# Optimization experiments

Measured on AMD Instinct MI355X. Metric: run time of the kernel, lower is better.

## Reference

```python
import jax, jax.numpy as jnp
import numpy as np

DIM = 1024
HEADS = 16


def setup_inputs() -> dict:
    key = jax.random.key(0)
    ks = jax.random.split(key, 8)
    b, n, d = 2, 2048, DIM
    x = jax.random.normal(ks[0], (b, n, d), dtype=jnp.float32)
    # Linear(dim, 3*dim, bias=False): weight stored as [dim, 3*dim] (pre-transposed)
    W_qkv = jax.random.normal(ks[1], (d, 3 * d), dtype=jnp.float32) * (d ** -0.5)
    # Linear(dim, dim) with bias
    W_out = jax.random.normal(ks[2], (d, d), dtype=jnp.float32) * (d ** -0.5)
    b_out = jnp.zeros((d,), dtype=jnp.float32)
    alpha = jnp.ones((1,), dtype=jnp.float32)
    beta = jnp.zeros((1,), dtype=jnp.float32) + 0.5  # nonzero so softmax path is exercised
    gamma = jnp.zeros((1,), dtype=jnp.float32) + 0.1
    return {"x": x, "W_qkv": W_qkv, "W_out": W_out, "b_out": b_out,
            "alpha": alpha, "beta": beta, "gamma": gamma}


def reference(x, W_qkv, W_out, b_out, alpha, beta, gamma):
    b, n, d = x.shape
    h = HEADS
    hd = d // h
    scale = d ** -0.5  # note: full dim, as in the original module
    qkv = x @ W_qkv  # [b, n, 3d]
    q, k, v = jnp.split(qkv, 3, axis=-1)
    # [b, n, d] -> [b, h, n, hd]
    to_heads = lambda t: t.reshape(b, n, h, hd).transpose(0, 2, 1, 3)
    q, k, v = to_heads(q), to_heads(k), to_heads(v)
    dots = jnp.einsum("bhqd,bhkd->bhqk", q, k) * scale  # [b, h, n, n]
    attn = (alpha[0] * jnp.eye(n, dtype=x.dtype)
            + beta[0] * jax.nn.softmax(dots, axis=-1)
            - gamma[0] / n)
    out = jnp.einsum("bhqk,bhkd->bhqd", attn, v)  # [b, h, n, hd]
    out = out.transpose(0, 2, 1, 3).reshape(b, n, d)
    return out @ W_out + b_out
```

## Files before the change

kernel.cpp:

```cpp
#include <hip/hip_runtime.h>
#include <hip/hip_bf16.h>

#define DEVI __device__ __forceinline__

typedef __attribute__((ext_vector_type(8))) short bf16x8;
typedef __attribute__((ext_vector_type(4))) short bf16x4;
typedef __attribute__((ext_vector_type(4))) float f32x4;

DEVI unsigned short f2bf(float f) {
    unsigned u = __float_as_uint(f);
    u += 0x7FFF + ((u >> 16) & 1);
    return (unsigned short)(u >> 16);
}
DEVI float bf2f(unsigned short h) {
    return __uint_as_float(((unsigned)h) << 16);
}
DEVI f32x4 mfma16(bf16x8 a, bf16x8 b, f32x4 c) {
    return __builtin_amdgcn_mfma_f32_16x16x32_bf16(a, b, c, 0, 0, 0);
}
DEVI void gload_lds16(const void* g, void* l) {
    __builtin_amdgcn_global_load_lds(
        (const __attribute__((address_space(1))) unsigned int*)g,
        (__attribute__((address_space(3))) unsigned int*)l, 16, 0, 0);
}

DEVI void wt_body(const float* __restrict__ W, unsigned short* __restrict__ Wt,
                  int N, int n0, int k0, float sc, int tid,
                  unsigned short (*T)[72])
{
#pragma unroll
    for (int j = 0; j < 4; ++j) {
        int idx = tid + j * 256;
        int kk = idx >> 4, c4 = (idx & 15) << 2;
        float4 v = *(const float4*)(W + (size_t)(k0 + kk) * N + n0 + c4);
        T[c4 + 0][kk] = f2bf(v.x * sc); T[c4 + 1][kk] = f2bf(v.y * sc);
        T[c4 + 2][kk] = f2bf(v.z * sc); T[c4 + 3][kk] = f2bf(v.w * sc);
    }
    __syncthreads();
#pragma unroll
    for (int j = 0; j < 4; ++j) {
        int idx = tid + j * 256;
        int n = idx >> 4, c4 = (idx & 15) << 2;
        *(bf16x4*)(Wt + (size_t)(n0 + n) * 1024 + k0 + c4) = *(bf16x4*)&T[n][c4];
    }
}

__global__ __launch_bounds__(256) void k_prep(
    const float* __restrict__ X, const float* __restrict__ Wqkv,
    const float* __restrict__ Wout,
    unsigned short* __restrict__ Xb, unsigned short* __restrict__ Wt1,
    unsigned short* __restrict__ Wt2)
{
    __shared__ unsigned short T[64][72];
    const int tid = threadIdx.x;
    const int bid = blockIdx.x;
    const float QSC = 1.4426950408889634f / 32.0f;
    if (bid < 1024) {
        int i = bid * 256 + tid;
#pragma unroll
        for (int j = 0; j < 4; ++j) {
            int idx = i + j * 262144;
            float4 v = *(const float4*)(X + (size_t)idx * 4);
            bf16x4 hv;
            hv[0] = (short)f2bf(v.x); hv[1] = (short)f2bf(v.y);
            hv[2] = (short)f2bf(v.z); hv[3] = (short)f2bf(v.w);
            *(bf16x4*)(Xb + (size_t)idx * 4) = hv;
        }
    } else if (bid < 1792) {
        int idx = bid - 1024;
        int n0 = (idx % 48) * 64, k0 = (idx / 48) * 64;
        wt_body(Wqkv, Wt1, 3072, n0, k0, (n0 < 1024) ? QSC : 1.0f, tid, T);
    } else {
        int idx = bid - 1792;
        int n0 = (idx & 15) * 64, k0 = (idx >> 4) * 64;
        wt_body(Wout, Wt2, 1024, n0, k0, 1.0f, tid, T);
    }
}

__global__ __launch_bounds__(256) void k_gemm1(
    const unsigned short* __restrict__ A, const unsigned short* __restrict__ B,
    unsigned short* __restrict__ C)
{
    __shared__ unsigned short As[128 * 64];
    __shared__ unsigned short Bs[128 * 64];
    const int tid = threadIdx.x, lane = tid & 63, wid = tid >> 6;
    const int wr = (wid >> 1) * 64, wc = (wid & 1) * 64;
    const int row0 = blockIdx.y * 128, col0 = blockIdx.x * 128;
    const int rsel = lane & 15, kgr = (lane >> 4) * 8;
    const int lr = lane >> 3, lc = (lane & 7) * 8;

    f32x4 acc[4][4];
#pragma unroll
    for (int i = 0; i < 4; ++i)
#pragma unroll
        for (int j = 0; j < 4; ++j) acc[i][j] = (f32x4){0.f, 0.f, 0.f, 0.f};

    for (int k0 = 0; k0 < 1024; k0 += 64) {
        __syncthreads();
#pragma unroll
        for (int i = 0; i < 4; ++i) {
            int rb = wid * 32 + i * 8;
            gload_lds16(A + (size_t)(row0 + rb + lr) * 1024 + k0 + lc, As + rb * 64);
            gload_lds16(B + (size_t)(col0 + rb + lr) * 1024 + k0 + lc, Bs + rb * 64);
        }
        __syncthreads();
#pragma unroll
        for (int ks = 0; ks < 2; ++ks) {
            bf16x8 a[4], b[4];
            int ko = ks * 32 + kgr;
#pragma unroll
            for (int mi = 0; mi < 4; ++mi)
                a[mi] = *(const bf16x8*)(As + (wr + mi * 16 + rsel) * 64 + ko);
#pragma unroll
            for (int nj = 0; nj < 4; ++nj)
                b[nj] = *(const bf16x8*)(Bs + (wc + nj * 16 + rsel) * 64 + ko);
#pragma unroll
            for (int mi = 0; mi < 4; ++mi)
#pragma unroll
                for (int nj = 0; nj < 4; ++nj)
                    acc[mi][nj] = mfma16(a[mi], b[nj], acc[mi][nj]);
        }
    }
    const int rbase = row0 + wr + ((lane >> 4) << 2);
    const int cbase = col0 + wc + rsel;
#pragma unroll
    for (int mi = 0; mi < 4; ++mi)
#pragma unroll
        for (int nj = 0; nj < 4; ++nj)
#pragma unroll
            for (int r = 0; r < 4; ++r)
                C[(size_t)(rbase + mi * 16 + r) * 3072 + cbase + nj * 16] =
                    f2bf(acc[mi][nj][r]);
}

__global__ __launch_bounds__(256) void k_vt(
    const unsigned short* __restrict__ qkv, unsigned short* __restrict__ Vt,
    float* __restrict__ vsum)
{
    __shared__ unsigned short T[64][72];
    __shared__ float ps[64];
    const int tid = threadIdx.x, lane = tid & 63, wid = tid >> 6;
    const int bh = blockIdx.y, b = bh >> 4, h = bh & 15;
    const int n0 = blockIdx.x * 64;
    const unsigned short* src = qkv + (size_t)(b * 2048 + n0) * 3072 + 2048 + h * 64;
#pragma unroll
    for (int j = 0; j < 2; ++j) {
        int idx = tid + j * 256;
        int n = idx >> 3, c8 = (idx & 7) << 3;
        *(bf16x8*)&T[n][c8] = *(const bf16x8*)(src + (size_t)n * 3072 + c8);
    }
    if (tid < 64) ps[tid] = 0.f;
    __syncthreads();
#pragma unroll
    for (int i = 0; i < 16; ++i) {
        int dv = wid * 16 + i;
        Vt[((size_t)bh * 64 + dv) * 2048 + n0 + lane] = T[lane][dv];
    }
    {
        const int col = tid & 63, qtr = tid >> 6;
        float s = 0.f;
#pragma unroll
        for (int i = 0; i < 16; ++i) s += bf2f(T[qtr * 16 + i][col]);
        atomicAdd(&ps[col], s);
        __syncthreads();
        if (tid < 64) atomicAdd(&vsum[bh * 64 + tid], ps[tid]);
    }
}

__global__ __launch_bounds__(256) void k_attn(
    const unsigned short* __restrict__ qkv, const unsigned short* __restrict__ Vt,
    const float* __restrict__ vsum,
    const float* __restrict__ alpha_p, const float* __restrict__ beta_p,
    const float* __restrict__ gamma_p,
    unsigned short* __restrict__ AO)
{
    __shared__ unsigned short Ks[2][64][64];
    __shared__ unsigned short Vs[2][64][64];
    __shared__ unsigned short Ps[4][32][64];
    const int tid = threadIdx.x, lane = tid & 63, wid = tid >> 6;
    const int swz = (blockIdx.x & 7) * 64 + (blockIdx.x >> 3);
    const int bh = swz >> 4, qtb = swz & 15;
    const int b = bh >> 4, h = bh & 15;
    const int q0 = qtb * 128;
    const int rsel = lane & 15, g = lane >> 4;
    const int g4 = g << 2;
    const int wq0 = wid * 32;
    const int r7 = rsel & 7;

    bf16x8 bq[2][2];
#pragma unroll
    for (int qt = 0; qt < 2; ++qt) {
        const unsigned short* qrow =
            qkv + (size_t)(b * 2048 + q0 + wq0 + qt * 16 + rsel) * 3072 + h * 64;
        bq[qt][0] = *(const bf16x8*)(qrow + g * 8);
        bq[qt][1] = *(const bf16x8*)(qrow + 32 + g * 8);
    }

    const int sr = lane >> 3;
    const int ss = (lane & 7) ^ sr;
    const int rb0 = wid * 16, rb1 = wid * 16 + 8;
    const unsigned short* kp0 = qkv + (size_t)(b * 2048) * 3072 + 1024 + h * 64
                              + (size_t)(rb0 + sr) * 3072 + ss * 8;
    const unsigned short* kp1 = kp0 + (size_t)8 * 3072;
    const unsigned short* vp0 = Vt + (size_t)bh * 64 * 2048
                              + (size_t)(rb0 + sr) * 2048 + ss * 8;
    const unsigned short* vp1 = vp0 + (size_t)8 * 2048;
    const size_t KADV = (size_t)64 * 3072;

    f32x4 o[2][4], ol[2];
#pragma unroll
    for (int qt = 0; qt < 2; ++qt) {
#pragma unroll
        for (int dj = 0; dj < 4; ++dj) o[qt][dj] = (f32x4){0.f, 0.f, 0.f, 0.f};
        ol[qt] = (f32x4){0.f, 0.f, 0.f, 0.f};
    }
    bf16x8 ones;
#pragma unroll
    for (int e = 0; e < 8; ++e) ones[e] = (short)0x3F80;

    gload_lds16(kp0, &Ks[0][rb0][0]); gload_lds16(kp1, &Ks[0][rb1][0]);
    gload_lds16(vp0, &Vs[0][rb0][0]); gload_lds16(vp1, &Vs[0][rb1][0]);
    kp0 += KADV; kp1 += KADV; vp0 += 64; vp1 += 64;
    asm volatile("s_waitcnt vmcnt(0)" ::: "memory");
    __syncthreads();

#define BODY(CUR, NXT, DOPF)                                                   \
    {                                                                          \
        if (DOPF) {                                                            \
            gload_lds16(kp0, &Ks[NXT][rb0][0]);                                \
            gload_lds16(kp1, &Ks[NXT][rb1][0]);                                \
            gload_lds16(vp0, &Vs[NXT][rb0][0]);                                \
            gload_lds16(vp1, &Vs[NXT][rb1][0]);                                \
            kp0 += KADV; kp1 += KADV; vp0 += 64; vp1 += 64;                    \
        }                                                                      \
        f32x4 s[2][4];                                                         \
        _Pragma("unroll")                                                      \
        for (int qt = 0; qt < 2; ++qt)                                         \
            _Pragma("unroll")                                                  \
            for (int kj = 0; kj < 4; ++kj)                                     \
                s[qt][kj] = (f32x4){0.f, 0.f, 0.f, 0.f};                       \
        __builtin_amdgcn_s_setprio(1);                                         \
        _Pragma("unroll")                                                      \
        for (int ks = 0; ks < 2; ++ks) {                                       \
            const int sl = ((ks * 4 + g) ^ r7) * 8;                            \
            bf16x8 ak[4];                                                      \
            _Pragma("unroll")                                                  \
            for (int kj = 0; kj < 4; ++kj)                                     \
                ak[kj] = *(const bf16x8*)(&Ks[CUR][kj * 16 + rsel][sl]);       \
            _Pragma("unroll")                                                  \
            for (int qt = 0; qt < 2; ++qt)                                     \
                _Pragma("unroll")                                              \
                for (int kj = 0; kj < 4; ++kj)                                 \
                    s[qt][kj] = mfma16(ak[kj], bq[qt][ks], s[qt][kj]);         \
        }                                                                      \
        __builtin_amdgcn_s_setprio(0);                                         \
        _Pragma("unroll")                                                      \
        for (int qt = 0; qt < 2; ++qt)                                         \
            _Pragma("unroll")                                                  \
            for (int kj = 0; kj < 4; ++kj) {                                   \
                float p0 = __builtin_amdgcn_exp2f(s[qt][kj][0]);               \
                float p1 = __builtin_amdgcn_exp2f(s[qt][kj][1]);               \
                float p2 = __builtin_amdgcn_exp2f(s[qt][kj][2]);               \
                float p3 = __builtin_amdgcn_exp2f(s[qt][kj][3]);               \
                union { __hip_bfloat162 h2[2]; uint2 u; } pk;                  \
                pk.h2[0] = __float22bfloat162_rn(make_float2(p0, p1));         \
                pk.h2[1] = __float22bfloat162_rn(make_float2(p2, p3));         \
                const int slot16 = (kj * 2 + (g >> 1)) ^ r7;                   \
                *(uint2*)(&Ps[wid][qt * 16 + rsel][slot16 * 8 + (g & 1) * 4])  \
                    = pk.u;                                                    \
            }                                                                  \
        __builtin_amdgcn_s_setprio(1);                                         \
        _Pragma("unroll")                                                      \
        for (int ks = 0; ks < 2; ++ks) {                                       \
            const int sl = ((ks * 4 + g) ^ r7) * 8;                            \
            bf16x8 pa0 = *(const bf16x8*)(&Ps[wid][rsel][sl]);                 \
            bf16x8 pa1 = *(const bf16x8*)(&Ps[wid][16 + rsel][sl]);            \
            bf16x8 vb[4];                                                      \
            _Pragma("unroll")                                                  \
            for (int dj = 0; dj < 4; ++dj)                                     \
                vb[dj] = *(const bf16x8*)(&Vs[CUR][dj * 16 + rsel][sl]);       \
            _Pragma("unroll")                                                  \
            for (int dj = 0; dj < 4; ++dj) {                                   \
                o[0][dj] = mfma16(pa0, vb[dj], o[0][dj]);                      \
                o[1][dj] = mfma16(pa1, vb[dj], o[1][dj]);                      \
            }                                                                  \
            ol[0] = mfma16(pa0, ones, ol[0]);                                  \
            ol[1] = mfma16(pa1, ones, ol[1]);                                  \
        }                                                                      \
        __builtin_amdgcn_s_setprio(0);                                         \
        asm volatile("s_waitcnt vmcnt(0)" ::: "memory");                       \
        __syncthreads();                                                       \
    }

#pragma unroll 1
    for (int i = 0; i < 16; ++i) {
        BODY(0, 1, true);
        BODY(1, 0, (i < 15));
    }
#undef BODY

    const float alpha = *alpha_p, beta = *beta_p;
    const float gn = (*gamma_p) / 2048.0f;
#pragma unroll
    for (int qt = 0; qt < 2; ++qt) {
        float linv[4];
#pragma unroll
        for (int r = 0; r < 4; ++r)
            linv[r] = beta / ol[qt][r];
#pragma unroll
        for (int dj = 0; dj < 4; ++dj)
#pragma unroll
            for (int r = 0; r < 4; ++r) {
                int qrow = q0 + wq0 + qt * 16 + g4 + r;
                int dv = dj * 16 + rsel;
                float ov = o[qt][dj][r] * linv[r];
                float vdiag = bf2f(qkv[(size_t)(b * 2048 + qrow) * 3072 + 2048 + h * 64 + dv]);
                float vs = vsum[bh * 64 + dv];
                float res = ov + alpha * vdiag - gn * vs;
                AO[(size_t)(b * 2048 + qrow) * 1024 + h * 64 + dv] = f2bf(res);
            }
    }
}

__global__ __launch_bounds__(256) void k_gemm2(
    const unsigned short* __restrict__ A, const unsigned short* __restrict__ B,
    const float* __restrict__ bias, float* __restrict__ Out)
{
    __shared__ unsigned short As[64 * 64];
    __shared__ unsigned short Bs[128 * 64];
    const int tid = threadIdx.x, lane = tid & 63, wid = tid >> 6;
    const int wr = (wid >> 1) * 32, wc = (wid & 1) * 64;
    const int row0 = blockIdx.y * 64, col0 = blockIdx.x * 128;
    const int rsel = lane & 15, kgr = (lane >> 4) * 8;
    const int lr = lane >> 3, lc = (lane & 7) * 8;

    f32x4 acc[2][4];
#pragma unroll
    for (int i = 0; i < 2; ++i)
#pragma unroll
        for (int j = 0; j < 4; ++j) acc[i][j] = (f32x4){0.f, 0.f, 0.f, 0.f};

    for (int k0 = 0; k0 < 1024; k0 += 64) {
        __syncthreads();
#pragma unroll
        for (int i = 0; i < 2; ++i) {
            int rb = wid * 8 + i * 32;
            gload_lds16(A + (size_t)(row0 + rb + lr) * 1024 + k0 + lc, As + rb * 64);
        }
#pragma unroll
        for (int i = 0; i < 4; ++i) {
            int rb = wid * 8 + i * 32;
            gload_lds16(B + (size_t)(col0 + rb + lr) * 1024 + k0 + lc, Bs + rb * 64);
        }
        __syncthreads();
#pragma unroll
        for (int ks = 0; ks < 2; ++ks) {
            bf16x8 a[2], b[4];
            int ko = ks * 32 + kgr;
#pragma unroll
            for (int mi = 0; mi < 2; ++mi)
                a[mi] = *(const bf16x8*)(As + (wr + mi * 16 + rsel) * 64 + ko);
#pragma unroll
            for (int nj = 0; nj < 4; ++nj)
                b[nj] = *(const bf16x8*)(Bs + (wc + nj * 16 + rsel) * 64 + ko);
#pragma unroll
            for (int mi = 0; mi < 2; ++mi)
#pragma unroll
                for (int nj = 0; nj < 4; ++nj)
                    acc[mi][nj] = mfma16(a[mi], b[nj], acc[mi][nj]);
        }
    }
    const int rbase = row0 + wr + ((lane >> 4) << 2);
    const int cbase = col0 + wc + rsel;
#pragma unroll
    for (int mi = 0; mi < 2; ++mi)
#pragma unroll
        for (int nj = 0; nj < 4; ++nj) {
            int gc = cbase + nj * 16;
            float bv = bias[gc];
#pragma unroll
            for (int r = 0; r < 4; ++r)
                Out[(size_t)(rbase + mi * 16 + r) * 1024 + gc] = acc[mi][nj][r] + bv;
        }
}

extern "C" void kernel_launch(void* const* d_in, const int* in_sizes, int n_in,
                              void* d_out, int out_size, void* d_ws, size_t ws_size,
                              hipStream_t stream) {
    const float* x     = (const float*)d_in[0];
    const float* Wqkv  = (const float*)d_in[1];
    const float* Wout  = (const float*)d_in[2];
    const float* bout  = (const float*)d_in[3];
    const float* alpha = (const float*)d_in[4];
    const float* beta  = (const float*)d_in[5];
    const float* gamma = (const float*)d_in[6];
    float* out = (float*)d_out;

    char* ws = (char*)d_ws;
    unsigned short* Xb  = (unsigned short*)(ws);
    unsigned short* Wt1 = (unsigned short*)(ws + 8388608);
    unsigned short* Wt2 = (unsigned short*)(ws + 14680064);
    unsigned short* qkv = (unsigned short*)(ws + 16777216);
    unsigned short* Vt  = (unsigned short*)(ws + 41943040);
    float* vsum         = (float*)(ws + 50331648);
    unsigned short* AO  = Xb;

    hipMemsetAsync(vsum, 0, 2048 * sizeof(float), stream);
    k_prep<<<2048, 256, 0, stream>>>(x, Wqkv, Wout, Xb, Wt1, Wt2);
    k_gemm1<<<dim3(24, 32), 256, 0, stream>>>(Xb, Wt1, qkv);
    k_vt<<<dim3(32, 32), 256, 0, stream>>>(qkv, Vt, vsum);
    k_attn<<<512, 256, 0, stream>>>(qkv, Vt, vsum, alpha, beta, gamma, AO);
    k_gemm2<<<dim3(8, 64), 256, 0, stream>>>(AO, Wt2, bout, out);
}
```

Measured before the change: 144.1 us.

## Process two KV tiles per barrier in attention and stage GEMM output via LDS

The attention loop now uses four K/V LDS buffers and handles two 64-key tiles per iteration. Both QK products are issued before both exp/PV phases, which halves the number of waitcnt+barrier points and gives more independent MFMA work to hide latency. Separately, the QKV GEMM epilogue writes its accumulators into padded shared memory and then stores 16-byte rows to global, replacing scattered 2-byte stores. The cost is doubled K/V shared memory and more live score registers, which may reduce occupancy.

```diff
diff --git a/kernel.cpp b/kernel.cpp
--- a/kernel.cpp
+++ b/kernel.cpp
@@ -81,8 +81,9 @@
     const unsigned short* __restrict__ A, const unsigned short* __restrict__ B,
     unsigned short* __restrict__ C)
 {
-    __shared__ unsigned short As[128 * 64];
-    __shared__ unsigned short Bs[128 * 64];
+    __shared__ unsigned short Sh[18432];
+    unsigned short* As = Sh;
+    unsigned short* Bs = Sh + 8192;
     const int tid = threadIdx.x, lane = tid & 63, wid = tid >> 6;
     const int wr = (wid >> 1) * 64, wc = (wid & 1) * 64;
     const int row0 = blockIdx.y * 128, col0 = blockIdx.x * 128;
@@ -121,16 +122,23 @@
                     acc[mi][nj] = mfma16(a[mi], b[nj], acc[mi][nj]);
         }
     }
-    const int rbase = row0 + wr + ((lane >> 4) << 2);
-    const int cbase = col0 + wc + rsel;
+    __syncthreads();
+    unsigned short (*wb)[72] = (unsigned short (*)[72])(Sh + wid * 4608);
+    const int g4 = (lane >> 4) << 2;
 #pragma unroll
     for (int mi = 0; mi < 4; ++mi)
 #pragma unroll
         for (int nj = 0; nj < 4; ++nj)
 #pragma unroll
             for (int r = 0; r < 4; ++r)
-                C[(size_t)(rbase + mi * 16 + r) * 3072 + cbase + nj * 16] =
-                    f2bf(acc[mi][nj][r]);
+                wb[mi * 16 + g4 + r][nj * 16 + rsel] = f2bf(acc[mi][nj][r]);
+#pragma unroll
+    for (int rr = 0; rr < 8; ++rr) {
+        int row = rr * 8 + (lane >> 3);
+        int c8 = (lane & 7) * 8;
+        bf16x8 v = *(const bf16x8*)&wb[row][c8];
+        *(bf16x8*)(C + (size_t)(row0 + wr + row) * 3072 + col0 + wc + c8) = v;
+    }
 }
 
 __global__ __launch_bounds__(256) void k_vt(
@@ -174,8 +182,8 @@
     const float* __restrict__ gamma_p,
     unsigned short* __restrict__ AO)
 {
-    __shared__ unsigned short Ks[2][64][64];
-    __shared__ unsigned short Vs[2][64][64];
+    __shared__ unsigned short Ks[4][64][64];
+    __shared__ unsigned short Vs[4][64][64];
     __shared__ unsigned short Ps[4][32][64];
     const int tid = threadIdx.x, lane = tid & 63, wid = tid >> 6;
     const int swz = (blockIdx.x & 7) * 64 + (blockIdx.x >> 3);
@@ -218,27 +226,26 @@
 #pragma unroll
     for (int e = 0; e < 8; ++e) ones[e] = (short)0x3F80;
 
-    gload_lds16(kp0, &Ks[0][rb0][0]); gload_lds16(kp1, &Ks[0][rb1][0]);
-    gload_lds16(vp0, &Vs[0][rb0][0]); gload_lds16(vp1, &Vs[0][rb1][0]);
-    kp0 += KADV; kp1 += KADV; vp0 += 64; vp1 += 64;
+#define STAGE(BUF)                                                             \
+    {                                                                          \
+        gload_lds16(kp0, &Ks[BUF][rb0][0]);                                    \
+        gload_lds16(kp1, &Ks[BUF][rb1][0]);                                    \
+        gload_lds16(vp0, &Vs[BUF][rb0][0]);                                    \
+        gload_lds16(vp1, &Vs[BUF][rb1][0]);                                    \
+        kp0 += KADV; kp1 += KADV; vp0 += 64; vp1 += 64;                        \
+    }
+
+    STAGE(0); STAGE(1);
     asm volatile("s_waitcnt vmcnt(0)" ::: "memory");
     __syncthreads();
 
-#define BODY(CUR, NXT, DOPF)                                                   \
+#define QK(CUR, S)                                                             \
     {                                                                          \
-        if (DOPF) {                                                            \
-            gload_lds16(kp0, &Ks[NXT][rb0][0]);                                \
-            gload_lds16(kp1, &Ks[NXT][rb1][0]);                                \
-            gload_lds16(vp0, &Vs[NXT][rb0][0]);                                \
-            gload_lds16(vp1, &Vs[NXT][rb1][0]);                                \
-            kp0 += KADV; kp1 += KADV; vp0 += 64; vp1 += 64;                    \
-        }                                                                      \
-        f32x4 s[2][4];                                                         \
         _Pragma("unroll")                                                      \
         for (int qt = 0; qt < 2; ++qt)                                         \
             _Pragma("unroll")                                                  \
             for (int kj = 0; kj < 4; ++kj)                                     \
-                s[qt][kj] = (f32x4){0.f, 0.f, 0.f, 0.f};                       \
+                S[qt][kj] = (f32x4){0.f, 0.f, 0.f, 0.f};                       \
         __builtin_amdgcn_s_setprio(1);                                         \
         _Pragma("unroll")                                                      \
         for (int ks = 0; ks < 2; ++ks) {                                       \
@@ -251,17 +258,21 @@
             for (int qt = 0; qt < 2; ++qt)                                     \
                 _Pragma("unroll")                                              \
                 for (int kj = 0; kj < 4; ++kj)                                 \
-                    s[qt][kj] = mfma16(ak[kj], bq[qt][ks], s[qt][kj]);         \
+                    S[qt][kj] = mfma16(ak[kj], bq[qt][ks], S[qt][kj]);         \
         }                                                                      \
         __builtin_amdgcn_s_setprio(0);                                         \
+    }
+
+#define EPV(CUR, S)                                                            \
+    {                                                                          \
         _Pragma("unroll")                                                      \
         for (int qt = 0; qt < 2; ++qt)                                         \
             _Pragma("unroll")                                                  \
             for (int kj = 0; kj < 4; ++kj) {                                   \
-                float p0 = __builtin_amdgcn_exp2f(s[qt][kj][0]);               \
-                float p1 = __builtin_amdgcn_exp2f(s[qt][kj][1]);               \
-                float p2 = __builtin_amdgcn_exp2f(s[qt][kj][2]);               \
-                float p3 = __builtin_amdgcn_exp2f(s[qt][kj][3]);               \
+                float p0 = __builtin_amdgcn_exp2f(S[qt][kj][0]);               \
+                float p1 = __builtin_amdgcn_exp2f(S[qt][kj][1]);               \
+                float p2 = __builtin_amdgcn_exp2f(S[qt][kj][2]);               \
+                float p3 = __builtin_amdgcn_exp2f(S[qt][kj][3]);               \
                 union { __hip_bfloat162 h2[2]; uint2 u; } pk;                  \
                 pk.h2[0] = __float22bfloat162_rn(make_float2(p0, p1));         \
                 pk.h2[1] = __float22bfloat162_rn(make_float2(p2, p3));         \
@@ -288,16 +299,29 @@
             ol[1] = mfma16(pa1, ones, ol[1]);                                  \
         }                                                                      \
         __builtin_amdgcn_s_setprio(0);                                         \
+    }
+
+#define PAIR(C0, C1, DOPF)                                                     \
+    {                                                                          \
+        f32x4 s0[2][4], s1[2][4];                                              \
+        if (DOPF) { STAGE(C0 ^ 2); STAGE(C1 ^ 2); }                            \
+        QK(C0, s0);                                                            \
+        QK(C1, s1);                                                            \
+        EPV(C0, s0);                                                           \
+        EPV(C1, s1);                                                           \
         asm volatile("s_waitcnt vmcnt(0)" ::: "memory");                       \
         __syncthreads();                                                       \
     }
 
 #pragma unroll 1
-    for (int i = 0; i < 16; ++i) {
-        BODY(0, 1, true);
-        BODY(1, 0, (i < 15));
-    }
-#undef BODY
+    for (int i = 0; i < 8; ++i) {
+        PAIR(0, 1, true);
+        PAIR(2, 3, (i < 7));
+    }
+#undef PAIR
+#undef EPV
+#undef QK
+#undef STAGE
 
     const float alpha = *alpha_p, beta = *beta_p;
     const float gn = (*gamma_p) / 2048.0f;
```

After: 143.0 us. About the same (-0.7%).
